# Kernel optimization log

Measured on AMD Instinct MI355X. Metric: run time of the kernel, lower is better.

The kernel has to match this reference:

```python
import jax, jax.numpy as jnp
import numpy as np

L, H, D, FF = 4, 16, 1024, 4   # nLayers, nHeads, embedDim, ffMult
EPS = 1e-5


def layernorm(x, g, b):
    mu = jnp.mean(x, axis=-1, keepdims=True)
    var = jnp.mean(jnp.square(x - mu), axis=-1, keepdims=True)
    return (x - mu) * jax.lax.rsqrt(var + EPS) * g + b


def setup_inputs() -> dict:
    key = jax.random.key(0)
    ks = jax.random.split(key, 4)
    B, N = 2, 2048
    s = 0.02
    return {
        "x": jax.random.normal(ks[0], (B, N, D), jnp.float32),
        "Wqkv": jax.random.normal(ks[1], (L, D, 3 * D), jnp.float32) * s,
        "bqkv": jnp.zeros((L, 3 * D), jnp.float32),
        "W1": jax.random.normal(ks[2], (L, D, FF * D), jnp.float32) * s,
        "b1": jnp.zeros((L, FF * D), jnp.float32),
        "W2": jax.random.normal(ks[3], (L, FF * D, D), jnp.float32) * s,
        "b2": jnp.zeros((L, D), jnp.float32),
        "g1": jnp.ones((L, D), jnp.float32),
        "be1": jnp.zeros((L, D), jnp.float32),
        "g2": jnp.ones((L, D), jnp.float32),
        "be2": jnp.zeros((L, D), jnp.float32),
    }


def reference(x, Wqkv, bqkv, W1, b1, W2, b2, g1, be1, g2, be2):
    B, N, _ = x.shape
    dh = D // H
    scale = D ** -0.5  # NOTE: module scales by embedDim**-0.5, not head_dim
    act = lambda t: jax.nn.gelu(t, approximate=False)
    for l in range(L):
        qkv = x @ Wqkv[l] + bqkv[l]                       # [B,N,3D]
        q, k, v = jnp.split(qkv, 3, axis=-1)
        q = q.reshape(B, N, H, dh)
        k = k.reshape(B, N, H, dh)
        v = v.reshape(B, N, H, dh)
        scores = jnp.einsum('bihd,bjhd->bhij', q, k) * scale  # [B,H,N,N]
        z = jax.nn.softmax(scores, axis=-1)
        o = jnp.einsum('bhij,bjhd->bihd', z, v).reshape(B, N, D)
        h = layernorm(o + x, g1[l], be1[l])               # post-LN residual 1
        f = act(h @ W1[l] + b1[l])
        f = act(f @ W2[l] + b2[l])                        # activation after 2nd linear too (as in Sequential)
        x = layernorm(f + h, g2[l], be2[l])               # post-LN residual 2
    return x
```

## Files before the change

### kernel.cpp

```cpp
#include <hip/hip_runtime.h>
#include <hip/hip_bf16.h>
#include <cmath>


typedef __attribute__((ext_vector_type(8))) short bf16x8;
typedef __attribute__((ext_vector_type(4))) float f32x4;
typedef __hip_bfloat16 bf16;

#define DEV static __device__ __forceinline__

DEV unsigned short f2b(float f) {
    bf16 h = __float2bfloat16(f);
    return *reinterpret_cast<unsigned short*>(&h);
}

DEV unsigned int pack_bf16(float lo, float hi) {
    return (unsigned int)f2b(lo) | ((unsigned int)f2b(hi) << 16);
}

DEV float b2f(unsigned short u) {
    unsigned int x = ((unsigned int)u) << 16;
    return *reinterpret_cast<float*>(&x);
}

DEV float gelu_fast(float x) {
    float u = 0.7978845608028654f * fmaf(0.044715f * x, x * x, x);
    u = fminf(fmaxf(u, -15.f), 15.f);
    float t = __builtin_amdgcn_exp2f(u * 2.8853900817779268f);
    float th = (t - 1.0f) * __builtin_amdgcn_rcpf(t + 1.0f);
    return 0.5f * x * (1.0f + th);
}

DEV void gload_lds16(const bf16* g, bf16* l) {
    __builtin_amdgcn_global_load_lds(
        (const __attribute__((address_space(1))) void*)g,
        (__attribute__((address_space(3))) void*)l, 16, 0, 0);
}

__global__ __launch_bounds__(256) void transpose_cast(const float* __restrict__ W,
                                                      bf16* __restrict__ Wt,
                                                      int K, int Nm) {
    __shared__ float tile[32][33];
    const int l = blockIdx.z;
    const float* Wl = W + (size_t)l * K * Nm;
    bf16* Wtl = Wt + (size_t)l * K * Nm;
    const int n0 = blockIdx.x * 32, k0 = blockIdx.y * 32;
    const int tx = threadIdx.x, ty = threadIdx.y;
#pragma unroll
    for (int i = 0; i < 4; ++i)
        tile[ty + 8 * i][tx] = Wl[(size_t)(k0 + ty + 8 * i) * Nm + n0 + tx];
    __syncthreads();
#pragma unroll
    for (int i = 0; i < 4; ++i)
        Wtl[(size_t)(n0 + ty + 8 * i) * K + k0 + tx] = __float2bfloat16(tile[tx][ty + 8 * i]);
}

__global__ __launch_bounds__(256) void cast_bf16_k(const float* __restrict__ in,
                                                   bf16* __restrict__ out, int n4) {
    int i = blockIdx.x * 256 + threadIdx.x;
    if (i >= n4) return;
    float4 v = reinterpret_cast<const float4*>(in)[i];
    ushort4 o = { f2b(v.x), f2b(v.y), f2b(v.z), f2b(v.w) };
    reinterpret_cast<ushort4*>(out)[i] = o;
}

template <int EPI>
__global__ __launch_bounds__(512, 2) void gemm256(const bf16* __restrict__ A,
                                                  const bf16* __restrict__ Bt,
                                                  const float* __restrict__ bias,
                                                  void* __restrict__ Cout,
                                                  void* __restrict__ Cout2,
                                                  int M, int Nm, int K,
                                                  int nbx, int ntiles, int Ktotal) {
    __shared__ bf16 As[2][256][64];
    __shared__ bf16 Bs[2][256][64];
    const int nwg = gridDim.x;
    int id = blockIdx.x;
    id = (id & 7) * (nwg >> 3) + (id >> 3);
    const int tile = id % ntiles, split = id / ntiles;
    const int m0 = (tile / nbx) * 256, n0 = (tile % nbx) * 256;
    const int kbase = split * K;
    const int t = threadIdx.x, w = t >> 6, lane = t & 63;
    const int wm = w >> 2, wn = w & 3;
    const int lr = lane & 15, lg = lane >> 4;
    const int srow = w * 8;
    const bf16* Ag = A + (size_t)(m0 + srow + (lane >> 3)) * Ktotal + kbase + (lane & 7) * 8;
    const bf16* Bg = Bt + (size_t)(n0 + srow + (lane >> 3)) * Ktotal + kbase + (lane & 7) * 8;

    f32x4 acc[8][4] = {};
    const int NT = K / 64;

#define STAGE256(kt, b)                                                          \
    {                                                                            \
        const size_t koff = (size_t)(kt) * 64;                                   \
        _Pragma("unroll")                                                        \
        for (int p = 0; p < 4; ++p)                                              \
            gload_lds16(Ag + (size_t)(p * 64) * Ktotal + koff,                   \
                        &As[b][p * 64 + srow][0]);                               \
        _Pragma("unroll")                                                        \
        for (int p = 0; p < 4; ++p)                                              \
            gload_lds16(Bg + (size_t)(p * 64) * Ktotal + koff,                   \
                        &Bs[b][p * 64 + srow][0]);                               \
    }

    STAGE256(0, 0);
    for (int kt = 0; kt < NT; ++kt) {
        const int buf = kt & 1;
        if (kt + 1 < NT) {
            STAGE256(kt + 1, buf ^ 1);
            asm volatile("s_waitcnt vmcnt(8)" ::: "memory");
        } else {
            asm volatile("s_waitcnt vmcnt(0)" ::: "memory");
        }
        __builtin_amdgcn_sched_barrier(0);
        __builtin_amdgcn_s_barrier();
        __builtin_amdgcn_sched_barrier(0);
        __builtin_amdgcn_s_setprio(1);
#pragma unroll
        for (int kk = 0; kk < 2; ++kk) {
            const int lk = kk * 32 + lg * 8;
            bf16x8 a[8], b[4];
#pragma unroll
            for (int m = 0; m < 8; ++m)
                a[m] = *reinterpret_cast<const bf16x8*>(&As[buf][wm * 128 + m * 16 + lr][lk]);
#pragma unroll
            for (int n = 0; n < 4; ++n)
                b[n] = *reinterpret_cast<const bf16x8*>(&Bs[buf][wn * 64 + n * 16 + lr][lk]);
#pragma unroll
            for (int m = 0; m < 8; ++m)
#pragma unroll
                for (int n = 0; n < 4; ++n)
                    acc[m][n] = __builtin_amdgcn_mfma_f32_16x16x32_bf16(a[m], b[n], acc[m][n], 0, 0, 0);
        }
        __builtin_amdgcn_s_setprio(0);
        __builtin_amdgcn_sched_barrier(0);
        __builtin_amdgcn_s_barrier();
        __builtin_amdgcn_sched_barrier(0);
    }
#undef STAGE256

    if (EPI == 3) {
        bf16* outp = (split < 2)
            ? (bf16*)Cout + (size_t)split * M * Nm
            : (bf16*)Cout2 + (size_t)(split - 2) * M * Nm;
#pragma unroll
        for (int n = 0; n < 4; ++n) {
            const int col = n0 + wn * 64 + n * 16 + lr;
#pragma unroll
            for (int m = 0; m < 8; ++m) {
                const int row = m0 + wm * 128 + m * 16 + lg * 4;
#pragma unroll
                for (int j = 0; j < 4; ++j)
                    outp[(size_t)(row + j) * Nm + col] = __float2bfloat16(acc[m][n][j]);
            }
        }
    } else if (EPI == 4 && n0 >= 2048) {
#pragma unroll
        for (int n = 0; n < 4; ++n) {
            const int col = n0 + wn * 64 + n * 16 + lr;
            const float bc = bias[col];
            const int vcol = col - 2048;
#pragma unroll
            for (int m = 0; m < 8; ++m) {
                const int row = m0 + wm * 128 + m * 16 + lg * 4;
                const int b = row >> 11, nn = row & 2047;
                ushort4 o = { f2b(acc[m][n][0] + bc), f2b(acc[m][n][1] + bc),
                              f2b(acc[m][n][2] + bc), f2b(acc[m][n][3] + bc) };
                *reinterpret_cast<ushort4*>(
                    (bf16*)Cout2 + ((size_t)(b * 1024 + vcol)) * 2048 + nn) = o;
            }
        }
    } else {
#pragma unroll
        for (int n = 0; n < 4; ++n) {
            const int col = n0 + wn * 64 + n * 16 + lr;
            const float bc = bias[col];
#pragma unroll
            for (int m = 0; m < 8; ++m) {
                const int row = m0 + wm * 128 + m * 16 + lg * 4;
#pragma unroll
                for (int j = 0; j < 4; ++j) {
                    float v = acc[m][n][j] + bc;
                    if (EPI == 1) v = gelu_fast(v);
                    reinterpret_cast<bf16*>(Cout)[(size_t)(row + j) * Nm + col] = __float2bfloat16(v);
                }
            }
        }
    }
}

__global__ __launch_bounds__(256) void attn_fwd(const bf16* __restrict__ qkv,
                                                const bf16* __restrict__ vtg,
                                                float* __restrict__ o, int N) {
    __shared__ bf16 Ks[2][64][72];
    __shared__ bf16 Vs[2][64][72];
    __shared__ bf16 Ps[4][32][72];
    const int nwg = gridDim.x, nbx = N / 128;
    int id = blockIdx.x;
    id = (id & 7) * (nwg >> 3) + (id >> 3);
    const int bh = id / nbx, b = bh >> 4, h = bh & 15;
    const int q0 = (id % nbx) * 128;
    const int t = threadIdx.x, w = t >> 6, lane = t & 63;
    const int lr = lane & 15, lg = lane >> 4;
    const bf16* base = qkv + (size_t)b * N * 3072;
    const bf16* vbase = vtg + (size_t)bh * 64 * N;

    bf16x8 qf[2][2];
#pragma unroll
    for (int rb = 0; rb < 2; ++rb) {
        const bf16* qp = base + (size_t)(q0 + w * 32 + rb * 16 + lr) * 3072 + h * 64 + lg * 8;
        qf[rb][0] = *reinterpret_cast<const bf16x8*>(qp);
        qf[rb][1] = *reinterpret_cast<const bf16x8*>(qp + 32);
    }

    float mrow[2] = { -INFINITY, -INFINITY };
    float lrow[2] = { 0.f, 0.f };
    f32x4 oacc[2][4] = {};
    const float scale2 = 0.03125f * 1.44269504088896340736f;
    const int srow = t >> 2, scolb = (t & 3) * 8;

    const bf16* kptr = base + (size_t)srow * 3072 + 1024 + h * 64 + scolb;
    const bf16* vptr = vbase + (size_t)srow * N + scolb;

    uint4 k0 = *reinterpret_cast<const uint4*>(kptr);
    uint4 k1 = *reinterpret_cast<const uint4*>(kptr + 32);
    uint4 v0 = *reinterpret_cast<const uint4*>(vptr);
    uint4 v1 = *reinterpret_cast<const uint4*>(vptr + 32);
    *reinterpret_cast<uint4*>(&Ks[0][srow][scolb])      = k0;
    *reinterpret_cast<uint4*>(&Ks[0][srow][scolb + 32]) = k1;
    *reinterpret_cast<uint4*>(&Vs[0][srow][scolb])      = v0;
    *reinterpret_cast<uint4*>(&Vs[0][srow][scolb + 32]) = v1;

    int cur = 0;
    for (int kv0 = 0; kv0 < N; kv0 += 64) {
        __syncthreads();
        const bool more = (kv0 + 64) < N;
        if (more) {
            const bf16* kn = kptr + (size_t)(kv0 + 64) * 3072;
            const bf16* vn = vptr + (kv0 + 64);
            k0 = *reinterpret_cast<const uint4*>(kn);
            k1 = *reinterpret_cast<const uint4*>(kn + 32);
            v0 = *reinterpret_cast<const uint4*>(vn);
            v1 = *reinterpret_cast<const uint4*>(vn + 32);
        }
        __builtin_amdgcn_sched_barrier(0);

        f32x4 st[2][4] = {};
#pragma unroll
        for (int f = 0; f < 2; ++f)
#pragma unroll
            for (int c = 0; c < 4; ++c) {
                bf16x8 ka = *reinterpret_cast<const bf16x8*>(&Ks[cur][c * 16 + lr][f * 32 + lg * 8]);
                st[0][c] = __builtin_amdgcn_mfma_f32_16x16x32_bf16(ka, qf[0][f], st[0][c], 0, 0, 0);
                st[1][c] = __builtin_amdgcn_mfma_f32_16x16x32_bf16(ka, qf[1][f], st[1][c], 0, 0, 0);
            }

#pragma unroll
        for (int rb = 0; rb < 2; ++rb) {
            float smax = st[rb][0][0];
#pragma unroll
            for (int c = 0; c < 4; ++c)
#pragma unroll
                for (int j = 0; j < 4; ++j) smax = fmaxf(smax, st[rb][c][j]);
            const float tilemax = smax * scale2;
            if (!__all(tilemax - mrow[rb] <= 11.0f)) {
                float tm = fmaxf(tilemax, __shfl_xor(tilemax, 16, 64));
                tm = fmaxf(tm, __shfl_xor(tm, 32, 64));
                const float mnew = fmaxf(mrow[rb], tm);
                const float al = __builtin_amdgcn_exp2f(mrow[rb] - mnew);
                mrow[rb] = mnew;
                lrow[rb] *= al;
#pragma unroll
                for (int c = 0; c < 4; ++c)
#pragma unroll
                    for (int j = 0; j < 4; ++j) oacc[rb][c][j] *= al;
            }
            float p[4][4];
            float psum = 0.f;
#pragma unroll
            for (int c = 0; c < 4; ++c)
#pragma unroll
                for (int j = 0; j < 4; ++j) {
                    p[c][j] = __builtin_amdgcn_exp2f(fmaf(st[rb][c][j], scale2, -mrow[rb]));
                    psum += p[c][j];
                }
            psum += __shfl_xor(psum, 16, 64);
            psum += __shfl_xor(psum, 32, 64);
            lrow[rb] += psum;
#pragma unroll
            for (int c = 0; c < 4; ++c) {
                uint2 pr = { pack_bf16(p[c][0], p[c][1]), pack_bf16(p[c][2], p[c][3]) };
                *reinterpret_cast<uint2*>(&Ps[w][rb * 16 + lr][c * 16 + lg * 4]) = pr;
            }
        }
        asm volatile("s_waitcnt lgkmcnt(0)" ::: "memory");
        __builtin_amdgcn_sched_barrier(0);

#pragma unroll
        for (int f = 0; f < 2; ++f) {
            bf16x8 pb0 = *reinterpret_cast<const bf16x8*>(&Ps[w][lr][f * 32 + lg * 8]);
            bf16x8 pb1 = *reinterpret_cast<const bf16x8*>(&Ps[w][16 + lr][f * 32 + lg * 8]);
#pragma unroll
            for (int c = 0; c < 4; ++c) {
                bf16x8 va = *reinterpret_cast<const bf16x8*>(&Vs[cur][c * 16 + lr][f * 32 + lg * 8]);
                oacc[0][c] = __builtin_amdgcn_mfma_f32_16x16x32_bf16(va, pb0, oacc[0][c], 0, 0, 0);
                oacc[1][c] = __builtin_amdgcn_mfma_f32_16x16x32_bf16(va, pb1, oacc[1][c], 0, 0, 0);
            }
        }

        if (more) {
            asm volatile("s_waitcnt vmcnt(0)" ::: "memory");
            __builtin_amdgcn_sched_barrier(0);
            *reinterpret_cast<uint4*>(&Ks[cur ^ 1][srow][scolb])      = k0;
            *reinterpret_cast<uint4*>(&Ks[cur ^ 1][srow][scolb + 32]) = k1;
            *reinterpret_cast<uint4*>(&Vs[cur ^ 1][srow][scolb])      = v0;
            *reinterpret_cast<uint4*>(&Vs[cur ^ 1][srow][scolb + 32]) = v1;
        }
        cur ^= 1;
    }

#pragma unroll
    for (int rb = 0; rb < 2; ++rb) {
        const float linv = 1.f / lrow[rb];
        float* op = o + ((size_t)b * N + q0 + w * 32 + rb * 16 + lr) * 1024 + h * 64;
#pragma unroll
        for (int c = 0; c < 4; ++c) {
            float4 v = { oacc[rb][c][0] * linv, oacc[rb][c][1] * linv,
                         oacc[rb][c][2] * linv, oacc[rb][c][3] * linv };
            *reinterpret_cast<float4*>(op + c * 16 + lg * 4) = v;
        }
    }
}

__global__ __launch_bounds__(256) void ln_res(const float* __restrict__ a,
                                              const float* __restrict__ r,
                                              const float* __restrict__ g,
                                              const float* __restrict__ be,
                                              float* __restrict__ y,
                                              bf16* __restrict__ yb) {
    const int row = blockIdx.x, t = threadIdx.x;
    float4 va = reinterpret_cast<const float4*>(a + (size_t)row * 1024)[t];
    float4 vr = reinterpret_cast<const float4*>(r + (size_t)row * 1024)[t];
    float v0 = va.x + vr.x, v1 = va.y + vr.y, v2 = va.z + vr.z, v3 = va.w + vr.w;
    float s1 = v0 + v1 + v2 + v3;
    float s2 = v0 * v0 + v1 * v1 + v2 * v2 + v3 * v3;
#pragma unroll
    for (int m = 1; m < 64; m <<= 1) {
        s1 += __shfl_xor(s1, m, 64);
        s2 += __shfl_xor(s2, m, 64);
    }
    __shared__ float ws1[4], ws2[4];
    if ((t & 63) == 0) { ws1[t >> 6] = s1; ws2[t >> 6] = s2; }
    __syncthreads();
    s1 = ws1[0] + ws1[1] + ws1[2] + ws1[3];
    s2 = ws2[0] + ws2[1] + ws2[2] + ws2[3];
    const float mean = s1 * (1.f / 1024.f);
    const float var = s2 * (1.f / 1024.f) - mean * mean;
    const float rstd = rsqrtf(var + 1e-5f);
    float4 gg = reinterpret_cast<const float4*>(g)[t];
    float4 bb = reinterpret_cast<const float4*>(be)[t];
    float o0 = (v0 - mean) * rstd * gg.x + bb.x;
    float o1 = (v1 - mean) * rstd * gg.y + bb.y;
    float o2 = (v2 - mean) * rstd * gg.z + bb.z;
    float o3 = (v3 - mean) * rstd * gg.w + bb.w;
    float4 out = { o0, o1, o2, o3 };
    reinterpret_cast<float4*>(y + (size_t)row * 1024)[t] = out;
    if (yb) {
        ushort4 ob = { f2b(o0), f2b(o1), f2b(o2), f2b(o3) };
        reinterpret_cast<ushort4*>(yb + (size_t)row * 1024)[t] = ob;
    }
}

__global__ __launch_bounds__(256) void ln_res_red4(const bf16* __restrict__ p0,
                                                   const bf16* __restrict__ p2,
                                                   const float* __restrict__ bias,
                                                   const float* __restrict__ r,
                                                   const float* __restrict__ g,
                                                   const float* __restrict__ be,
                                                   float* __restrict__ y,
                                                   bf16* __restrict__ yb,
                                                   size_t stride) {
    const int row = blockIdx.x, t = threadIdx.x;
    const size_t off = (size_t)row * 1024 + t * 4;
    float4 bb4 = reinterpret_cast<const float4*>(bias)[t];
    float s0 = bb4.x, s1v = bb4.y, s2v = bb4.z, s3 = bb4.w;
#pragma unroll
    for (int k = 0; k < 2; ++k) {
        ushort4 va = *reinterpret_cast<const ushort4*>(p0 + k * stride + off);
        s0 += b2f(va.x); s1v += b2f(va.y); s2v += b2f(va.z); s3 += b2f(va.w);
        ushort4 vb = *reinterpret_cast<const ushort4*>(p2 + k * stride + off);
        s0 += b2f(vb.x); s1v += b2f(vb.y); s2v += b2f(vb.z); s3 += b2f(vb.w);
    }
    float4 vr = reinterpret_cast<const float4*>(r + (size_t)row * 1024)[t];
    float v0 = gelu_fast(s0) + vr.x;
    float v1 = gelu_fast(s1v) + vr.y;
    float v2 = gelu_fast(s2v) + vr.z;
    float v3 = gelu_fast(s3) + vr.w;
    float s1 = v0 + v1 + v2 + v3;
    float s2 = v0 * v0 + v1 * v1 + v2 * v2 + v3 * v3;
#pragma unroll
    for (int m = 1; m < 64; m <<= 1) {
        s1 += __shfl_xor(s1, m, 64);
        s2 += __shfl_xor(s2, m, 64);
    }
    __shared__ float ws1[4], ws2[4];
    if ((t & 63) == 0) { ws1[t >> 6] = s1; ws2[t >> 6] = s2; }
    __syncthreads();
    s1 = ws1[0] + ws1[1] + ws1[2] + ws1[3];
    s2 = ws2[0] + ws2[1] + ws2[2] + ws2[3];
    const float mean = s1 * (1.f / 1024.f);
    const float var = s2 * (1.f / 1024.f) - mean * mean;
    const float rstd = rsqrtf(var + 1e-5f);
    float4 gg = reinterpret_cast<const float4*>(g)[t];
    float4 bb = reinterpret_cast<const float4*>(be)[t];
    float o0 = (v0 - mean) * rstd * gg.x + bb.x;
    float o1 = (v1 - mean) * rstd * gg.y + bb.y;
    float o2 = (v2 - mean) * rstd * gg.z + bb.z;
    float o3 = (v3 - mean) * rstd * gg.w + bb.w;
    float4 out = { o0, o1, o2, o3 };
    reinterpret_cast<float4*>(y + (size_t)row * 1024)[t] = out;
    ushort4 ob = { f2b(o0), f2b(o1), f2b(o2), f2b(o3) };
    reinterpret_cast<ushort4*>(yb + (size_t)row * 1024)[t] = ob;
}

extern "C" void kernel_launch(void* const* d_in, const int* in_sizes, int n_in,
                              void* d_out, int out_size, void* d_ws, size_t ws_size,
                              hipStream_t stream) {
    const float* x_in = (const float*)d_in[0];
    const float* Wqkv = (const float*)d_in[1];
    const float* bqkv = (const float*)d_in[2];
    const float* W1   = (const float*)d_in[3];
    const float* b1   = (const float*)d_in[4];
    const float* W2   = (const float*)d_in[5];
    const float* b2   = (const float*)d_in[6];
    const float* g1   = (const float*)d_in[7];
    const float* be1  = (const float*)d_in[8];
    const float* g2   = (const float*)d_in[9];
    const float* be2  = (const float*)d_in[10];

    const int Bv = 2, N = 2048, L = 4, Hh = 16;
    const int R = Bv * N;

    char* p = (char*)d_ws;
    auto alloc = [&](size_t bytes) { char* r = p; p += (bytes + 255) & ~(size_t)255; return r; };
    bf16*  Wqkvt = (bf16*)alloc((size_t)L * 3072 * 1024 * 2);
    bf16*  W1t   = (bf16*)alloc((size_t)L * 4096 * 1024 * 2);
    bf16*  W2t   = (bf16*)alloc((size_t)L * 1024 * 4096 * 2);
    bf16*  xb    = (bf16*)alloc((size_t)R * 1024 * 2);
    bf16*  qkvb  = (bf16*)alloc((size_t)R * 3072 * 2);
    float* obuf  = (float*)alloc((size_t)R * 1024 * 4);
    float* hbuf  = (float*)alloc((size_t)R * 1024 * 4);
    bf16*  hb    = (bf16*)alloc((size_t)R * 1024 * 2);
    bf16*  f1b   = (bf16*)alloc((size_t)R * 4096 * 2);
    float* xcur  = (float*)alloc((size_t)R * 1024 * 4);
    bf16*  vtg   = (bf16*)hbuf;
    bf16*  part0 = (bf16*)obuf;
    bf16*  part2 = (bf16*)qkvb;

    transpose_cast<<<dim3(3072 / 32, 1024 / 32, L), dim3(32, 8), 0, stream>>>(Wqkv, Wqkvt, 1024, 3072);
    transpose_cast<<<dim3(4096 / 32, 1024 / 32, L), dim3(32, 8), 0, stream>>>(W1, W1t, 1024, 4096);
    transpose_cast<<<dim3(1024 / 32, 4096 / 32, L), dim3(32, 8), 0, stream>>>(W2, W2t, 4096, 1024);
    cast_bf16_k<<<(R * 1024 / 4 + 255) / 256, 256, 0, stream>>>(x_in, xb, R * 1024 / 4);

    const float* xres = x_in;
    for (int l = 0; l < L; ++l) {
        gemm256<4><<<(R / 256) * (3072 / 256), 512, 0, stream>>>(
            xb, Wqkvt + (size_t)l * 3072 * 1024, bqkv + l * 3072, qkvb, vtg,
            R, 3072, 1024, 3072 / 256, (R / 256) * (3072 / 256), 1024);
        attn_fwd<<<(N / 128) * (Bv * Hh), 256, 0, stream>>>(qkvb, vtg, obuf, N);
        ln_res<<<R, 256, 0, stream>>>(obuf, xres, g1 + l * 1024, be1 + l * 1024, hbuf, hb);
        gemm256<1><<<(R / 256) * (4096 / 256), 512, 0, stream>>>(
            hb, W1t + (size_t)l * 4096 * 1024, b1 + l * 4096, f1b, nullptr,
            R, 4096, 1024, 4096 / 256, (R / 256) * (4096 / 256), 1024);
        gemm256<3><<<(R / 256) * (1024 / 256) * 4, 512, 0, stream>>>(
            f1b, W2t + (size_t)l * 1024 * 4096, nullptr, part0, part2,
            R, 1024, 1024, 1024 / 256, (R / 256) * (1024 / 256), 4096);
        float* xn = (l == L - 1) ? (float*)d_out : xcur;
        ln_res_red4<<<R, 256, 0, stream>>>(part0, part2, b2 + l * 1024, hbuf,
                                           g2 + l * 1024, be2 + l * 1024, xn, xb,
                                           (size_t)R * 1024);
        xres = xn;
    }
}
```

Baseline: 1.063 ms.

## Split attention over two KV halves and merge partials in residual LayerNorm

```diff
diff --git a/kernel.cpp b/kernel.cpp
--- a/kernel.cpp
+++ b/kernel.cpp
@@ -191,15 +191,19 @@
 
 __global__ __launch_bounds__(256) void attn_fwd(const bf16* __restrict__ qkv,
                                                 const bf16* __restrict__ vtg,
-                                                float* __restrict__ o, int N) {
-    __shared__ bf16 Ks[2][64][72];
-    __shared__ bf16 Vs[2][64][72];
-    __shared__ bf16 Ps[4][32][72];
+                                                float* __restrict__ opart,
+                                                float2* __restrict__ ml,
+                                                int N, size_t halfstride) {
+    __shared__ bf16 Ks[2][64][68];
+    __shared__ bf16 Vs[2][64][68];
+    __shared__ bf16 Ps[4][32][68];
     const int nwg = gridDim.x, nbx = N / 128;
     int id = blockIdx.x;
     id = (id & 7) * (nwg >> 3) + (id >> 3);
-    const int bh = id / nbx, b = bh >> 4, h = bh & 15;
-    const int q0 = (id % nbx) * 128;
+    const int bh = id / (nbx * 2), rem = id % (nbx * 2);
+    const int q0 = (rem >> 1) * 128, half = rem & 1;
+    const int b = bh >> 4, h = bh & 15;
+    const int kvbase = half * (N / 2), NKV = N / 2;
     const int t = threadIdx.x, w = t >> 6, lane = t & 63;
     const int lr = lane & 15, lg = lane >> 4;
     const bf16* base = qkv + (size_t)b * N * 3072;
@@ -219,8 +223,8 @@
     const float scale2 = 0.03125f * 1.44269504088896340736f;
     const int srow = t >> 2, scolb = (t & 3) * 8;
 
-    const bf16* kptr = base + (size_t)srow * 3072 + 1024 + h * 64 + scolb;
-    const bf16* vptr = vbase + (size_t)srow * N + scolb;
+    const bf16* kptr = base + (size_t)(kvbase + srow) * 3072 + 1024 + h * 64 + scolb;
+    const bf16* vptr = vbase + (size_t)srow * N + kvbase + scolb;
 
     uint4 k0 = *reinterpret_cast<const uint4*>(kptr);
     uint4 k1 = *reinterpret_cast<const uint4*>(kptr + 32);
@@ -232,9 +236,9 @@
     *reinterpret_cast<uint4*>(&Vs[0][srow][scolb + 32]) = v1;
 
     int cur = 0;
-    for (int kv0 = 0; kv0 < N; kv0 += 64) {
+    for (int kv0 = 0; kv0 < NKV; kv0 += 64) {
         __syncthreads();
-        const bool more = (kv0 + 64) < N;
+        const bool more = (kv0 + 64) < NKV;
         if (more) {
             const bf16* kn = kptr + (size_t)(kv0 + 64) * 3072;
             const bf16* vn = vptr + (kv0 + 64);
@@ -319,89 +323,56 @@
         cur ^= 1;
     }
 
+    float* obase = opart + half * halfstride;
 #pragma unroll
     for (int rb = 0; rb < 2; ++rb) {
+        const int q = q0 + w * 32 + rb * 16 + lr;
         const float linv = 1.f / lrow[rb];
-        float* op = o + ((size_t)b * N + q0 + w * 32 + rb * 16 + lr) * 1024 + h * 64;
+        float* op = obase + ((size_t)b * N + q) * 1024 + h * 64;
 #pragma unroll
         for (int c = 0; c < 4; ++c) {
             float4 v = { oacc[rb][c][0] * linv, oacc[rb][c][1] * linv,
                          oacc[rb][c][2] * linv, oacc[rb][c][3] * linv };
             *reinterpret_cast<float4*>(op + c * 16 + lg * 4) = v;
         }
-    }
-}
-
-__global__ __launch_bounds__(256) void ln_res(const float* __restrict__ a,
-                                              const float* __restrict__ r,
-                                              const float* __restrict__ g,
-                                              const float* __restrict__ be,
-                                              float* __restrict__ y,
-                                              bf16* __restrict__ yb) {
+        if (lg == 0) {
+            float2 v = { mrow[rb], lrow[rb] };
+            ml[(size_t)half * 65536 + (size_t)bh * 2048 + q] = v;
+        }
+    }
+}
+
+__global__ __launch_bounds__(256) void ln_res_att(const float* __restrict__ opart,
+                                                  const float2* __restrict__ ml,
+                                                  size_t halfstride,
+                                                  const float* __restrict__ r,
+                                                  const float* __restrict__ g,
+                                                  const float* __restrict__ be,
+                                                  float* __restrict__ y,
+                                                  bf16* __restrict__ yb) {
     const int row = blockIdx.x, t = threadIdx.x;
-    float4 va = reinterpret_cast<const float4*>(a + (size_t)row * 1024)[t];
+    const int b = row >> 11, q = row & 2047, h = t >> 4;
+    const int bh = b * 16 + h;
+    float2 mla = ml[(size_t)bh * 2048 + q];
+    float2 mlb = ml[65536 + (size_t)bh * 2048 + q];
+    const float m = fmaxf(mla.x, mlb.x);
+    const float wa = mla.y * __builtin_amdgcn_exp2f(mla.x - m);
+    const float wb = mlb.y * __builtin_amdgcn_exp2f(mlb.x - m);
+    const float rw = 1.f / (wa + wb);
+    const float ca = wa * rw, cb = wb * rw;
+    float4 va = reinterpret_cast<const float4*>(opart + (size_t)row * 1024)[t];
+    float4 vb = reinterpret_cast<const float4*>(opart + halfstride + (size_t)row * 1024)[t];
     float4 vr = reinterpret_cast<const float4*>(r + (size_t)row * 1024)[t];
-    float v0 = va.x + vr.x, v1 = va.y + vr.y, v2 = va.z + vr.z, v3 = va.w + vr.w;
+    float v0 = ca * va.x + cb * vb.x + vr.x;
+    float v1 = ca * va.y + cb * vb.y + vr.y;
+    float v2 = ca * va.z + cb * vb.z + vr.z;
+    float v3 = ca * va.w + cb * vb.w + vr.w;
     float s1 = v0 + v1 + v2 + v3;
     float s2 = v0 * v0 + v1 * v1 + v2 * v2 + v3 * v3;
 #pragma unroll
-    for (int m = 1; m < 64; m <<= 1) {
-        s1 += __shfl_xor(s1, m, 64);
-        s2 += __shfl_xor(s2, m, 64);
-    }
-    __shared__ float ws1[4], ws2[4];
-    if ((t & 63) == 0) { ws1[t >> 6] = s1; ws2[t >> 6] = s2; }
-    __syncthreads();
-    s1 = ws1[0] + ws1[1] + ws1[2] + ws1[3];
-    s2 = ws2[0] + ws2[1] + ws2[2] + ws2[3];
-    const float mean = s1 * (1.f / 1024.f);
-    const float var = s2 * (1.f / 1024.f) - mean * mean;
-    const float rstd = rsqrtf(var + 1e-5f);
-    float4 gg = reinterpret_cast<const float4*>(g)[t];
-    float4 bb = reinterpret_cast<const float4*>(be)[t];
-    float o0 = (v0 - mean) * rstd * gg.x + bb.x;
-    float o1 = (v1 - mean) * rstd * gg.y + bb.y;
-    float o2 = (v2 - mean) * rstd * gg.z + bb.z;
-    float o3 = (v3 - mean) * rstd * gg.w + bb.w;
-    float4 out = { o0, o1, o2, o3 };
-    reinterpret_cast<float4*>(y + (size_t)row * 1024)[t] = out;
-    if (yb) {
-        ushort4 ob = { f2b(o0), f2b(o1), f2b(o2), f2b(o3) };
-        reinterpret_cast<ushort4*>(yb + (size_t)row * 1024)[t] = ob;
-    }
-}
-
-__global__ __launch_bounds__(256) void ln_res_red4(const bf16* __restrict__ p0,
-                                                   const bf16* __restrict__ p2,
-                                                   const float* __restrict__ bias,
-                                                   const float* __restrict__ r,
-                                                   const float* __restrict__ g,
-                                                   const float* __restrict__ be,
-                                                   float* __restrict__ y,
-                                                   bf16* __restrict__ yb,
-                                                   size_t stride) {
-    const int row = blockIdx.x, t = threadIdx.x;
-    const size_t off = (size_t)row * 1024 + t * 4;
-    float4 bb4 = reinterpret_cast<const float4*>(bias)[t];
-    float s0 = bb4.x, s1v = bb4.y, s2v = bb4.z, s3 = bb4.w;
-#pragma unroll
-    for (int k = 0; k < 2; ++k) {
-        ushort4 va = *reinterpret_cast<const ushort4*>(p0 + k * stride + off);
-        s0 += b2f(va.x); s1v += b2f(va.y); s2v += b2f(va.z); s3 += b2f(va.w);
-        ushort4 vb = *reinterpret_cast<const ushort4*>(p2 + k * stride + off);
-        s0 += b2f(vb.x); s1v += b2f(vb.y); s2v += b2f(vb.z); s3 += b2f(vb.w);
-    }
-    float4 vr = reinterpret_cast<const float4*>(r + (size_t)row * 1024)[t];
-    float v0 = gelu_fast(s0) + vr.x;
-    float v1 = gelu_fast(s1v) + vr.y;
-    float v2 = gelu_fast(s2v) + vr.z;
-    float v3 = gelu_fast(s3) + vr.w;
-    float s1 = v0 + v1 + v2 + v3;
-    float s2 = v0 * v0 + v1 * v1 + v2 * v2 + v3 * v3;
-#pragma unroll
-    for (int m = 1; m < 64; m <<= 1) {
-        s1 += __shfl_xor(s1, m, 64);
-        s2 += __shfl_xor(s2, m, 64);
+    for (int mm = 1; mm < 64; mm <<= 1) {
+        s1 += __shfl_xor(s1, mm, 64);
+        s2 += __shfl_xor(s2, mm, 64);
     }
     __shared__ float ws1[4], ws2[4];
     if ((t & 63) == 0) { ws1[t >> 6] = s1; ws2[t >> 6] = s2; }
@@ -423,6 +394,58 @@
     reinterpret_cast<ushort4*>(yb + (size_t)row * 1024)[t] = ob;
 }
 
+__global__ __launch_bounds__(256) void ln_res_red4(const bf16* __restrict__ p0,
+                                                   const bf16* __restrict__ p2,
+                                                   const float* __restrict__ bias,
+                                                   const float* __restrict__ r,
+                                                   const float* __restrict__ g,
+                                                   const float* __restrict__ be,
+                                                   float* __restrict__ y,
+                                                   bf16* __restrict__ yb,
+                                                   size_t stride) {
+    const int row = blockIdx.x, t = threadIdx.x;
+    const size_t off = (size_t)row * 1024 + t * 4;
+    float4 bb4 = reinterpret_cast<const float4*>(bias)[t];
+    float s0 = bb4.x, s1v = bb4.y, s2v = bb4.z, s3 = bb4.w;
+#pragma unroll
+    for (int k = 0; k < 2; ++k) {
+        ushort4 va = *reinterpret_cast<const ushort4*>(p0 + k * stride + off);
+        s0 += b2f(va.x); s1v += b2f(va.y); s2v += b2f(va.z); s3 += b2f(va.w);
+        ushort4 vb = *reinterpret_cast<const ushort4*>(p2 + k * stride + off);
+        s0 += b2f(vb.x); s1v += b2f(vb.y); s2v += b2f(vb.z); s3 += b2f(vb.w);
+    }
+    float4 vr = reinterpret_cast<const float4*>(r + (size_t)row * 1024)[t];
+    float v0 = gelu_fast(s0) + vr.x;
+    float v1 = gelu_fast(s1v) + vr.y;
+    float v2 = gelu_fast(s2v) + vr.z;
+    float v3 = gelu_fast(s3) + vr.w;
+    float s1 = v0 + v1 + v2 + v3;
+    float s2 = v0 * v0 + v1 * v1 + v2 * v2 + v3 * v3;
+#pragma unroll
+    for (int m = 1; m < 64; m <<= 1) {
+        s1 += __shfl_xor(s1, m, 64);
+        s2 += __shfl_xor(s2, m, 64);
+    }
+    __shared__ float ws1[4], ws2[4];
+    if ((t & 63) == 0) { ws1[t >> 6] = s1; ws2[t >> 6] = s2; }
+    __syncthreads();
+    s1 = ws1[0] + ws1[1] + ws1[2] + ws1[3];
+    s2 = ws2[0] + ws2[1] + ws2[2] + ws2[3];
+    const float mean = s1 * (1.f / 1024.f);
+    const float var = s2 * (1.f / 1024.f) - mean * mean;
+    const float rstd = rsqrtf(var + 1e-5f);
+    float4 gg = reinterpret_cast<const float4*>(g)[t];
+    float4 bb = reinterpret_cast<const float4*>(be)[t];
+    float o0 = (v0 - mean) * rstd * gg.x + bb.x;
+    float o1 = (v1 - mean) * rstd * gg.y + bb.y;
+    float o2 = (v2 - mean) * rstd * gg.z + bb.z;
+    float o3 = (v3 - mean) * rstd * gg.w + bb.w;
+    float4 out = { o0, o1, o2, o3 };
+    reinterpret_cast<float4*>(y + (size_t)row * 1024)[t] = out;
+    ushort4 ob = { f2b(o0), f2b(o1), f2b(o2), f2b(o3) };
+    reinterpret_cast<ushort4*>(yb + (size_t)row * 1024)[t] = ob;
+}
+
 extern "C" void kernel_launch(void* const* d_in, const int* in_sizes, int n_in,
                               void* d_out, int out_size, void* d_ws, size_t ws_size,
                               hipStream_t stream) {
@@ -453,7 +476,9 @@
     bf16*  hb    = (bf16*)alloc((size_t)R * 1024 * 2);
     bf16*  f1b   = (bf16*)alloc((size_t)R * 4096 * 2);
     float* xcur  = (float*)alloc((size_t)R * 1024 * 4);
+    float2* mlb  = (float2*)alloc((size_t)2 * 65536 * 8);
     bf16*  vtg   = (bf16*)hbuf;
+    float* opart = (float*)f1b;
     bf16*  part0 = (bf16*)obuf;
     bf16*  part2 = (bf16*)qkvb;
 
@@ -467,8 +492,10 @@
         gemm256<4><<<(R / 256) * (3072 / 256), 512, 0, stream>>>(
             xb, Wqkvt + (size_t)l * 3072 * 1024, bqkv + l * 3072, qkvb, vtg,
             R, 3072, 1024, 3072 / 256, (R / 256) * (3072 / 256), 1024);
-        attn_fwd<<<(N / 128) * (Bv * Hh), 256, 0, stream>>>(qkvb, vtg, obuf, N);
-        ln_res<<<R, 256, 0, stream>>>(obuf, xres, g1 + l * 1024, be1 + l * 1024, hbuf, hb);
+        attn_fwd<<<(N / 128) * (Bv * Hh) * 2, 256, 0, stream>>>(
+            qkvb, vtg, opart, mlb, N, (size_t)R * 1024);
+        ln_res_att<<<R, 256, 0, stream>>>(opart, mlb, (size_t)R * 1024, xres,
+                                          g1 + l * 1024, be1 + l * 1024, hbuf, hb);
         gemm256<1><<<(R / 256) * (4096 / 256), 512, 0, stream>>>(
             hb, W1t + (size_t)l * 4096 * 1024, b1 + l * 4096, f1b, nullptr,
             R, 4096, 1024, 4096 / 256, (R / 256) * (4096 / 256), 1024);
```

Result: no change. 1.084 ms (+1.9%).

## Add finely pipelined 256x256 GEMM variant for FFN layers

Applied to the files above, without the earlier changes.

```diff
diff --git a/kernel.cpp b/kernel.cpp
--- a/kernel.cpp
+++ b/kernel.cpp
@@ -139,22 +139,7 @@
     }
 #undef STAGE256
 
-    if (EPI == 3) {
-        bf16* outp = (split < 2)
-            ? (bf16*)Cout + (size_t)split * M * Nm
-            : (bf16*)Cout2 + (size_t)(split - 2) * M * Nm;
-#pragma unroll
-        for (int n = 0; n < 4; ++n) {
-            const int col = n0 + wn * 64 + n * 16 + lr;
-#pragma unroll
-            for (int m = 0; m < 8; ++m) {
-                const int row = m0 + wm * 128 + m * 16 + lg * 4;
-#pragma unroll
-                for (int j = 0; j < 4; ++j)
-                    outp[(size_t)(row + j) * Nm + col] = __float2bfloat16(acc[m][n][j]);
-            }
-        }
-    } else if (EPI == 4 && n0 >= 2048) {
+    if (EPI == 4 && n0 >= 2048) {
 #pragma unroll
         for (int n = 0; n < 4; ++n) {
             const int col = n0 + wn * 64 + n * 16 + lr;
@@ -182,6 +167,169 @@
                 for (int j = 0; j < 4; ++j) {
                     float v = acc[m][n][j] + bc;
                     if (EPI == 1) v = gelu_fast(v);
+                    reinterpret_cast<bf16*>(Cout)[(size_t)(row + j) * Nm + col] = __float2bfloat16(v);
+                }
+            }
+        }
+    }
+}
+
+template <int EPI>
+__global__ __launch_bounds__(512, 2) void gemm256p(const bf16* __restrict__ A,
+                                                   const bf16* __restrict__ Bt,
+                                                   const float* __restrict__ bias,
+                                                   void* __restrict__ Cout,
+                                                   void* __restrict__ Cout2,
+                                                   int M, int Nm, int K,
+                                                   int nbx, int ntiles, int Ktotal) {
+    __shared__ bf16 As[2][256][64];
+    __shared__ bf16 Bs[2][256][64];
+    const int nwg = gridDim.x;
+    int id = blockIdx.x;
+    id = (id & 7) * (nwg >> 3) + (id >> 3);
+    const int tile = id % ntiles, split = id / ntiles;
+    const int m0 = (tile / nbx) * 256, n0 = (tile % nbx) * 256;
+    const int kbase = split * K;
+    const int t = threadIdx.x, lane = t & 63;
+    const int w = t >> 6;
+    const int wm = w >> 2, wn = w & 3;
+    const int lr = lane & 15, lg = lane >> 4;
+    const int srowt = t >> 3;
+    const int scol = (t & 7) * 8;
+    const int gcol = (((t & 7) ^ ((t >> 3) & 7)) * 8);
+    const bf16* Ag = A + (size_t)(m0 + srowt) * Ktotal + kbase + gcol;
+    const bf16* Bg = Bt + (size_t)(n0 + srowt) * Ktotal + kbase + gcol;
+    const int cidx0 = ((lg) ^ (lr & 7)) * 8;
+    const int cidx1 = ((4 + lg) ^ (lr & 7)) * 8;
+
+    f32x4 acc[8][4] = {};
+    const int NT = K / 64;
+
+#define STAGEH(h, kt, d)                                                         \
+    {                                                                            \
+        const size_t koff = (size_t)(kt) * 64;                                   \
+        _Pragma("unroll")                                                        \
+        for (int p = 0; p < 2; ++p) {                                            \
+            const int roff = ((h) & 1) * 128 + p * 64;                           \
+            if ((h) < 2)                                                         \
+                gload_lds16(Ag + (size_t)roff * Ktotal + koff,                   \
+                            &As[d][roff + srowt][scol]);                         \
+            else                                                                 \
+                gload_lds16(Bg + (size_t)roff * Ktotal + koff,                   \
+                            &Bs[d][roff + srowt][scol]);                         \
+        }                                                                        \
+    }
+
+    STAGEH(0, 0, 0); STAGEH(1, 0, 0); STAGEH(2, 0, 0); STAGEH(3, 0, 0);
+
+    for (int kt = 0; kt < NT; ++kt) {
+        const int d = kt & 1;
+        const bool more = (kt + 1) < NT;
+        asm volatile("s_waitcnt vmcnt(0)" ::: "memory");
+        __builtin_amdgcn_sched_barrier(0);
+        __builtin_amdgcn_s_barrier();
+        __builtin_amdgcn_sched_barrier(0);
+
+        bf16x8 a[8], b[4];
+
+        if (more) STAGEH(0, kt + 1, d ^ 1);
+#pragma unroll
+        for (int m = 0; m < 8; ++m)
+            a[m] = *reinterpret_cast<const bf16x8*>(&As[d][wm * 128 + m * 16 + lr][cidx0]);
+        b[0] = *reinterpret_cast<const bf16x8*>(&Bs[d][wn * 64 + lr][cidx0]);
+        b[1] = *reinterpret_cast<const bf16x8*>(&Bs[d][wn * 64 + 16 + lr][cidx0]);
+        __builtin_amdgcn_sched_barrier(0);
+        __builtin_amdgcn_s_barrier();
+        asm volatile("s_waitcnt lgkmcnt(0)" ::: "memory");
+        __builtin_amdgcn_sched_barrier(0);
+        __builtin_amdgcn_s_setprio(1);
+#pragma unroll
+        for (int m = 0; m < 8; ++m) {
+            acc[m][0] = __builtin_amdgcn_mfma_f32_16x16x32_bf16(a[m], b[0], acc[m][0], 0, 0, 0);
+            acc[m][1] = __builtin_amdgcn_mfma_f32_16x16x32_bf16(a[m], b[1], acc[m][1], 0, 0, 0);
+        }
+        __builtin_amdgcn_s_setprio(0);
+        __builtin_amdgcn_sched_barrier(0);
+
+        if (more) STAGEH(1, kt + 1, d ^ 1);
+        b[2] = *reinterpret_cast<const bf16x8*>(&Bs[d][wn * 64 + 32 + lr][cidx0]);
+        b[3] = *reinterpret_cast<const bf16x8*>(&Bs[d][wn * 64 + 48 + lr][cidx0]);
+        __builtin_amdgcn_sched_barrier(0);
+        __builtin_amdgcn_s_barrier();
+        asm volatile("s_waitcnt lgkmcnt(0)" ::: "memory");
+        __builtin_amdgcn_sched_barrier(0);
+        __builtin_amdgcn_s_setprio(1);
+#pragma unroll
+        for (int m = 0; m < 8; ++m) {
+            acc[m][2] = __builtin_amdgcn_mfma_f32_16x16x32_bf16(a[m], b[2], acc[m][2], 0, 0, 0);
+            acc[m][3] = __builtin_amdgcn_mfma_f32_16x16x32_bf16(a[m], b[3], acc[m][3], 0, 0, 0);
+        }
+        __builtin_amdgcn_s_setprio(0);
+        __builtin_amdgcn_sched_barrier(0);
+
+        if (more) STAGEH(2, kt + 1, d ^ 1);
+#pragma unroll
+        for (int m = 0; m < 8; ++m)
+            a[m] = *reinterpret_cast<const bf16x8*>(&As[d][wm * 128 + m * 16 + lr][cidx1]);
+        b[0] = *reinterpret_cast<const bf16x8*>(&Bs[d][wn * 64 + lr][cidx1]);
+        b[1] = *reinterpret_cast<const bf16x8*>(&Bs[d][wn * 64 + 16 + lr][cidx1]);
+        __builtin_amdgcn_sched_barrier(0);
+        __builtin_amdgcn_s_barrier();
+        asm volatile("s_waitcnt lgkmcnt(0)" ::: "memory");
+        __builtin_amdgcn_sched_barrier(0);
+        __builtin_amdgcn_s_setprio(1);
+#pragma unroll
+        for (int m = 0; m < 8; ++m) {
+            acc[m][0] = __builtin_amdgcn_mfma_f32_16x16x32_bf16(a[m], b[0], acc[m][0], 0, 0, 0);
+            acc[m][1] = __builtin_amdgcn_mfma_f32_16x16x32_bf16(a[m], b[1], acc[m][1], 0, 0, 0);
+        }
+        __builtin_amdgcn_s_setprio(0);
+        __builtin_amdgcn_sched_barrier(0);
+
+        if (more) STAGEH(3, kt + 1, d ^ 1);
+        b[2] = *reinterpret_cast<const bf16x8*>(&Bs[d][wn * 64 + 32 + lr][cidx1]);
+        b[3] = *reinterpret_cast<const bf16x8*>(&Bs[d][wn * 64 + 48 + lr][cidx1]);
+        __builtin_amdgcn_sched_barrier(0);
+        __builtin_amdgcn_s_barrier();
+        asm volatile("s_waitcnt lgkmcnt(0)" ::: "memory");
+        __builtin_amdgcn_sched_barrier(0);
+        __builtin_amdgcn_s_setprio(1);
+#pragma unroll
+        for (int m = 0; m < 8; ++m) {
+            acc[m][2] = __builtin_amdgcn_mfma_f32_16x16x32_bf16(a[m], b[2], acc[m][2], 0, 0, 0);
+            acc[m][3] = __builtin_amdgcn_mfma_f32_16x16x32_bf16(a[m], b[3], acc[m][3], 0, 0, 0);
+        }
+        __builtin_amdgcn_s_setprio(0);
+        __builtin_amdgcn_sched_barrier(0);
+    }
+#undef STAGEH
+
+    if (EPI == 3) {
+        bf16* outp = (split < 2)
+            ? (bf16*)Cout + (size_t)split * M * Nm
+            : (bf16*)Cout2 + (size_t)(split - 2) * M * Nm;
+#pragma unroll
+        for (int n = 0; n < 4; ++n) {
+            const int col = n0 + wn * 64 + n * 16 + lr;
+#pragma unroll
+            for (int m = 0; m < 8; ++m) {
+                const int row = m0 + wm * 128 + m * 16 + lg * 4;
+#pragma unroll
+                for (int j = 0; j < 4; ++j)
+                    outp[(size_t)(row + j) * Nm + col] = __float2bfloat16(acc[m][n][j]);
+            }
+        }
+    } else {
+#pragma unroll
+        for (int n = 0; n < 4; ++n) {
+            const int col = n0 + wn * 64 + n * 16 + lr;
+            const float bc = bias[col];
+#pragma unroll
+            for (int m = 0; m < 8; ++m) {
+                const int row = m0 + wm * 128 + m * 16 + lg * 4;
+#pragma unroll
+                for (int j = 0; j < 4; ++j) {
+                    float v = gelu_fast(acc[m][n][j] + bc);
                     reinterpret_cast<bf16*>(Cout)[(size_t)(row + j) * Nm + col] = __float2bfloat16(v);
                 }
             }
@@ -469,10 +617,10 @@
             R, 3072, 1024, 3072 / 256, (R / 256) * (3072 / 256), 1024);
         attn_fwd<<<(N / 128) * (Bv * Hh), 256, 0, stream>>>(qkvb, vtg, obuf, N);
         ln_res<<<R, 256, 0, stream>>>(obuf, xres, g1 + l * 1024, be1 + l * 1024, hbuf, hb);
-        gemm256<1><<<(R / 256) * (4096 / 256), 512, 0, stream>>>(
+        gemm256p<1><<<(R / 256) * (4096 / 256), 512, 0, stream>>>(
             hb, W1t + (size_t)l * 4096 * 1024, b1 + l * 4096, f1b, nullptr,
             R, 4096, 1024, 4096 / 256, (R / 256) * (4096 / 256), 1024);
-        gemm256<3><<<(R / 256) * (1024 / 256) * 4, 512, 0, stream>>>(
+        gemm256p<3><<<(R / 256) * (1024 / 256) * 4, 512, 0, stream>>>(
             f1b, W2t + (size_t)l * 1024 * 4096, nullptr, part0, part2,
             R, 1024, 1024, 1024 / 256, (R / 256) * (1024 / 256), 4096);
         float* xn = (l == L - 1) ? (float*)d_out : xcur;
```

Result: faster. 1.039 ms (-2.3%).
